# Performance work log

Measured on AMD Instinct MI355X. Metric: run time of the kernel, lower is better.

## Reference

```python
import jax, jax.numpy as jnp
import numpy as np

B, S, D, H, HD, F, V = 16, 512, 256, 8, 32, 682, 32000
EPS = 1.1920928955078125e-07


def rmsnorm(x, w):
    return x * jax.lax.rsqrt(jnp.mean(x * x, axis=-1, keepdims=True) + EPS) * w


def rope(x, cos, sin):
    # interleaved RoPE: even/odd lanes rotated pairwise, re-interleaved
    xe, xo = x[..., ::2], x[..., 1::2]
    return jnp.stack([xe * cos - xo * sin, xe * sin + xo * cos], axis=-1).reshape(x.shape)


def setup_inputs() -> dict:
    key = jax.random.key(0)
    ks = jax.random.split(key, 12)
    def n(k, shape, s=0.02):
        return jax.random.normal(k, shape, jnp.float32) * s
    pos = jnp.arange(S, dtype=jnp.float32)
    inv = 1.0 / (10000.0 ** (jnp.arange(0, HD, 2, dtype=jnp.float32) / HD))
    ang = pos[:, None] * inv[None, :]                      # [S, HD/2]
    cos_tab = jnp.repeat(jnp.cos(ang), 2, axis=-1)         # [S, HD]
    sin_tab = jnp.repeat(jnp.sin(ang), 2, axis=-1)
    mask = jnp.tril(jnp.ones((S, S), jnp.int32))[None, None]  # causal [1,1,S,S]
    return dict(
        emb=n(ks[0], (V, D)),
        pos_emb=n(ks[1], (S, D)),
        attn_norm_w=jnp.ones((D,), jnp.float32),
        wq=n(ks[2], (D, D)), bq=jnp.zeros((D,), jnp.float32),
        wk=n(ks[3], (HD, D)), bk=jnp.zeros((HD,), jnp.float32),
        wv=n(ks[4], (D, D)), bv=jnp.zeros((D,), jnp.float32),
        cos_tab=cos_tab, sin_tab=sin_tab,
        ffn_norm_w=jnp.ones((D,), jnp.float32),
        w_gate=n(ks[5], (F, D)), b_gate=jnp.zeros((F,), jnp.float32),
        w_up=n(ks[6], (F, D)), b_up=jnp.zeros((F,), jnp.float32),
        w_down=n(ks[7], (D, F)), b_down=jnp.zeros((D,), jnp.float32),
        tok_ids=jax.random.randint(ks[8], (B, S), 0, V, jnp.int64),
        mask=mask,
    )


def reference(emb, pos_emb, attn_norm_w, wq, bq, wk, bk, wv, bv, cos_tab, sin_tab,
              ffn_norm_w, w_gate, b_gate, w_up, b_up, w_down, b_down, tok_ids, mask):
    h = emb[tok_ids] + pos_emb                                   # [B,S,D]
    x = rmsnorm(h, attn_norm_w)
    # faithful to trace: direct view [B,S,D] -> [B,H,S,HD] (no transpose)
    q = (x @ wq.T + bq).reshape(B, H, S, HD)
    k = (x @ wk.T + bk)[:, None]                                 # [B,1,S,HD] single KV head
    v = (x @ wv.T + bv).reshape(B, H, S, HD)
    cos = cos_tab[:S, ::2][None, None]                           # [1,1,S,HD/2]
    sin = sin_tab[:S, ::2][None, None]
    qr = rope(q, cos, sin)
    kr = rope(k, cos, sin)[:, 0]                                 # [B,S,HD]
    scores = jnp.einsum('bhsd,btd->bhst', qr, kr) / jnp.sqrt(jnp.float32(HD))
    scores = jnp.where(mask == 0, -jnp.inf, scores)
    attn = jax.nn.softmax(scores, axis=-1)
    o = jnp.einsum('bhst,bhtd->bhsd', attn, v).reshape(B, S, D)
    h2 = o + h
    x2 = rmsnorm(h2, ffn_norm_w)
    g = x2 @ w_gate.T + b_gate
    g = g * jax.nn.sigmoid(g)                                    # SiLU gate
    up = x2 @ w_up.T + b_up
    out = (g * up) @ w_down.T + b_down
    # faithful to trace: residual uses post-norm activation x2, not h2
    return out + x2
```

## Files before the change

### kernel.cpp

```cpp
#include <hip/hip_runtime.h>
#include <hip/hip_bf16.h>
#include <cstddef>
#include <cstdint>

constexpr int Bb = 16, Ss = 512, Dd = 256, Hh = 8, HDd = 32, Ff = 682;
constexpr int FKp = 704;
constexpr float EPSf = 1.1920928955078125e-07f;

typedef short bf8v __attribute__((ext_vector_type(8)));
typedef float f4 __attribute__((ext_vector_type(4)));
using bf16 = __hip_bfloat16;

__device__ inline f4 MFMA(bf8v a, bf8v b, f4 c) {
  return __builtin_amdgcn_mfma_f32_16x16x32_bf16(a, b, c, 0, 0, 0);
}

__device__ __forceinline__ void gl_lds16(const bf16* g, bf16* l) {
  __builtin_amdgcn_global_load_lds(
      (const __attribute__((address_space(1))) unsigned int*)(g),
      (__attribute__((address_space(3))) unsigned int*)(l), 16, 0, 0);
}

__global__ __launch_bounds__(256) void k_prep(
    const float* __restrict__ wq, const float* __restrict__ wk,
    const float* __restrict__ wv, const float* __restrict__ wg,
    const float* __restrict__ wu, const float* __restrict__ wd,
    bf16* __restrict__ dqkv, bf16* __restrict__ dgate,
    bf16* __restrict__ dup, bf16* __restrict__ ddown,
    const float* __restrict__ emb, const float* __restrict__ pos,
    const int* __restrict__ tok, const float* __restrict__ w,
    bf16* __restrict__ hb, bf16* __restrict__ xb)
{
  const int b = blockIdx.x, tid = threadIdx.x;
  if (b < 640) {
    const int idx = b * 256 + tid;
    const int row = idx >> 8, col = idx & 255;
    float v;
    if (row < 256)      v = wq[(size_t)row * 256 + col];
    else if (row < 288) v = wk[(size_t)(row - 256) * 256 + col];
    else if (row < 544) v = wv[(size_t)(row - 288) * 256 + col];
    else                v = 0.f;
    dqkv[idx] = __float2bfloat16(v);
  } else if (b < 2176) {
    const bool isg = b < 1408;
    const int idx = (b - (isg ? 640 : 1408)) * 256 + tid;
    const int row = idx >> 8, col = idx & 255;
    const float* src = isg ? wg : wu;
    float v = (row < Ff) ? src[(size_t)row * 256 + col] : 0.f;
    (isg ? dgate : dup)[idx] = __float2bfloat16(v);
  } else if (b < 2880) {
    const int idx = (b - 2176) * 256 + tid;
    const int row = idx / FKp, col = idx - row * FKp;
    float v = (col < Ff) ? wd[(size_t)row * Ff + col] : 0.f;
    ddown[idx] = __float2bfloat16(v);
  } else {
    const int row = b - 2880;
    const int s = row & (Ss - 1);
    const int t = tok[row];
    float v = emb[(size_t)t * Dd + tid] + pos[(size_t)s * Dd + tid];
    float ss = v * v;
    #pragma unroll
    for (int off = 32; off > 0; off >>= 1) ss += __shfl_down(ss, off);
    __shared__ float red[4];
    if ((tid & 63) == 0) red[tid >> 6] = ss;
    __syncthreads();
    const float tot = red[0] + red[1] + red[2] + red[3];
    const float r = rsqrtf(tot * (1.0f / Dd) + EPSf);
    const size_t o = (size_t)row * Dd + tid;
    hb[o] = __float2bfloat16(v);
    xb[o] = __float2bfloat16(v * r * w[tid]);
  }
}

__global__ __launch_bounds__(256) void k_add_norm(
    const bf16* __restrict__ a, const bf16* __restrict__ hb,
    const float* __restrict__ w, bf16* __restrict__ x2b)
{
  const int row = blockIdx.x;
  const int tid = threadIdx.x;
  const size_t off = (size_t)row * Dd + tid;
  const float v = __bfloat162float(a[off]) + __bfloat162float(hb[off]);
  float ss = v * v;
  #pragma unroll
  for (int o = 32; o > 0; o >>= 1) ss += __shfl_down(ss, o);
  __shared__ float red[4];
  if ((tid & 63) == 0) red[tid >> 6] = ss;
  __syncthreads();
  const float tot = red[0] + red[1] + red[2] + red[3];
  const float r = rsqrtf(tot * (1.0f / Dd) + EPSf);
  x2b[off] = __float2bfloat16(v * r * w[tid]);
}

__global__ __launch_bounds__(256) void k_qkv(
    const bf16* __restrict__ A, const bf16* __restrict__ W,
    const float* __restrict__ bias0, const float* __restrict__ bias1,
    const float* __restrict__ bias2,
    const float* __restrict__ cost, const float* __restrict__ sint,
    bf16* __restrict__ ob0, bf16* __restrict__ ob1, bf16* __restrict__ vt)
{
  __shared__ bf16 As[128 * 64];
  __shared__ bf16 Bs[64 * 64];
  const int tid = threadIdx.x, lane = tid & 63, wv = tid >> 6;
  const int l15 = lane & 15, lg = lane >> 4;
  const int m0 = blockIdx.x * 128, n0 = blockIdx.y * 64;
  const int wr = (wv >> 1) * 64, wc = (wv & 1) * 32;
  const int sr8 = lane >> 3, slot = lane & 7;

  f4 acc[4][2];
  #pragma unroll
  for (int i = 0; i < 4; i++)
    #pragma unroll
    for (int j = 0; j < 2; j++) acc[i][j] = (f4){0.f, 0.f, 0.f, 0.f};

  for (int ks = 0; ks < 4; ks++) {
    const int k0 = ks * 64;
    #pragma unroll
    for (int i = 0; i < 4; i++) {
      const int row = wv * 32 + i * 8 + sr8;
      gl_lds16(&A[(size_t)(m0 + row) * 256 + k0 + slot * 8],
               &As[(wv * 32 + i * 8) * 64]);
    }
    #pragma unroll
    for (int i = 0; i < 2; i++) {
      const int row = wv * 16 + i * 8 + sr8;
      gl_lds16(&W[(size_t)(n0 + row) * 256 + k0 + slot * 8],
               &Bs[(wv * 16 + i * 8) * 64]);
    }
    __syncthreads();
    #pragma unroll
    for (int kk = 0; kk < 64; kk += 32) {
      bf8v af[4], bw[2];
      #pragma unroll
      for (int mi = 0; mi < 4; mi++)
        af[mi] = *(const bf8v*)&As[(wr + mi * 16 + l15) * 64 + kk + lg * 8];
      #pragma unroll
      for (int ni = 0; ni < 2; ni++)
        bw[ni] = *(const bf8v*)&Bs[(wc + ni * 16 + l15) * 64 + kk + lg * 8];
      #pragma unroll
      for (int mi = 0; mi < 4; mi++)
        #pragma unroll
        for (int ni = 0; ni < 2; ni++)
          acc[mi][ni] = MFMA(af[mi], bw[ni], acc[mi][ni]);
    }
    if (ks < 3) __syncthreads();
  }

  #pragma unroll
  for (int mi = 0; mi < 4; mi++) {
    #pragma unroll
    for (int ni = 0; ni < 2; ni++) {
      const int nbase = n0 + wc + ni * 16;
      const int n = nbase + l15;
      if (nbase < 288) {
        #pragma unroll
        for (int r = 0; r < 4; r++) {
          const int m = m0 + wr + mi * 16 + lg * 4 + r;
          float vb2 = acc[mi][ni][r] + (nbase < 256 ? bias0[n] : bias1[n - 256]);
          int s, hd;
          if (nbase < 256) { const int flat = ((m & 511) << 8) + n; s = (flat >> 5) & 511; hd = n & 31; }
          else             { s = m & 511; hd = n - 256; }
          const float c = cost[s * 32 + hd], sn = sint[s * 32 + hd];
          const float other = __shfl_xor(vb2, 1);
          const float res = (n & 1) ? (other * sn + vb2 * c) : (vb2 * c - other * sn);
          if (nbase < 256) ob0[(size_t)m * 256 + n] = __float2bfloat16(res);
          else             ob1[(size_t)m * 32 + hd] = __float2bfloat16(res);
        }
      } else if (nbase < 544) {
        const int rel = n - 288;
        const int hd = rel & 31, rq = rel >> 5;
        const int mb = m0 + wr + mi * 16 + lg * 4;
        const int b = mb >> 9;
        const float bv = bias2[rel];
        #pragma unroll
        for (int r = 0; r < 4; r++) {
          const int s = (mb + r) & 511;
          const int hh2 = s >> 6;
          const int s4 = ((s & 63) << 3) + rq;
          vt[((size_t)(b * Hh + hh2) * HDd + hd) * Ss + s4] =
              __float2bfloat16(acc[mi][ni][r] + bv);
        }
      }
    }
  }
}

__global__ __launch_bounds__(256) void k_ffn(
    const bf16* __restrict__ A, const bf16* __restrict__ Wg,
    const bf16* __restrict__ Wu,
    const float* __restrict__ bg, const float* __restrict__ bu,
    bf16* __restrict__ out)
{
  __shared__ bf16 As[128 * 64];
  __shared__ bf16 Gs[64 * 64];
  __shared__ bf16 Us[64 * 64];
  const int tid = threadIdx.x, lane = tid & 63, wv = tid >> 6;
  const int l15 = lane & 15, lg = lane >> 4;
  const int m0 = blockIdx.x * 128, n0 = blockIdx.y * 64;
  const int wr = (wv >> 1) * 64, wc = (wv & 1) * 32;
  const int sr8 = lane >> 3, slot = lane & 7;

  f4 accg[4][2], accu[4][2];
  #pragma unroll
  for (int i = 0; i < 4; i++)
    #pragma unroll
    for (int j = 0; j < 2; j++) {
      accg[i][j] = (f4){0.f, 0.f, 0.f, 0.f};
      accu[i][j] = (f4){0.f, 0.f, 0.f, 0.f};
    }

  for (int ks = 0; ks < 4; ks++) {
    const int k0 = ks * 64;
    #pragma unroll
    for (int i = 0; i < 4; i++) {
      const int row = wv * 32 + i * 8 + sr8;
      gl_lds16(&A[(size_t)(m0 + row) * 256 + k0 + slot * 8],
               &As[(wv * 32 + i * 8) * 64]);
    }
    #pragma unroll
    for (int i = 0; i < 2; i++) {
      const int row = wv * 16 + i * 8 + sr8;
      gl_lds16(&Wg[(size_t)(n0 + row) * 256 + k0 + slot * 8],
               &Gs[(wv * 16 + i * 8) * 64]);
      gl_lds16(&Wu[(size_t)(n0 + row) * 256 + k0 + slot * 8],
               &Us[(wv * 16 + i * 8) * 64]);
    }
    __syncthreads();
    #pragma unroll
    for (int kk = 0; kk < 64; kk += 32) {
      bf8v af[4], bgf[2], buf[2];
      #pragma unroll
      for (int mi = 0; mi < 4; mi++)
        af[mi] = *(const bf8v*)&As[(wr + mi * 16 + l15) * 64 + kk + lg * 8];
      #pragma unroll
      for (int ni = 0; ni < 2; ni++) {
        bgf[ni] = *(const bf8v*)&Gs[(wc + ni * 16 + l15) * 64 + kk + lg * 8];
        buf[ni] = *(const bf8v*)&Us[(wc + ni * 16 + l15) * 64 + kk + lg * 8];
      }
      #pragma unroll
      for (int mi = 0; mi < 4; mi++)
        #pragma unroll
        for (int ni = 0; ni < 2; ni++) {
          accg[mi][ni] = MFMA(af[mi], bgf[ni], accg[mi][ni]);
          accu[mi][ni] = MFMA(af[mi], buf[ni], accu[mi][ni]);
        }
    }
    if (ks < 3) __syncthreads();
  }

  #pragma unroll
  for (int ni = 0; ni < 2; ni++) {
    const int n = n0 + wc + ni * 16 + l15;
    const float bgv = (n < Ff) ? bg[n] : 0.f;
    const float buv = (n < Ff) ? bu[n] : 0.f;
    #pragma unroll
    for (int mi = 0; mi < 4; mi++) {
      #pragma unroll
      for (int r = 0; r < 4; r++) {
        const int m = m0 + wr + mi * 16 + lg * 4 + r;
        float res = 0.f;
        if (n < Ff) {
          const float gv = accg[mi][ni][r] + bgv;
          const float uv = accu[mi][ni][r] + buv;
          res = gv / (1.f + __expf(-gv)) * uv;
        }
        out[(size_t)m * FKp + n] = __float2bfloat16(res);
      }
    }
  }
}

__global__ __launch_bounds__(256) void k_down(
    const bf16* __restrict__ A, const bf16* __restrict__ W,
    const float* __restrict__ bias, const bf16* __restrict__ resid,
    float* __restrict__ out)
{
  __shared__ bf16 As[64 * 64];
  __shared__ bf16 Bs[64 * 64];
  const int tid = threadIdx.x, lane = tid & 63, wv = tid >> 6;
  const int l15 = lane & 15, lg = lane >> 4;
  const int m0 = blockIdx.x * 64, n0 = blockIdx.y * 64;
  const int wr = (wv >> 1) * 32, wc = (wv & 1) * 32;
  const int sr8 = lane >> 3, slot = lane & 7;

  f4 acc[2][2];
  #pragma unroll
  for (int i = 0; i < 2; i++)
    #pragma unroll
    for (int j = 0; j < 2; j++) acc[i][j] = (f4){0.f, 0.f, 0.f, 0.f};

  for (int ks = 0; ks < 11; ks++) {
    const int k0 = ks * 64;
    #pragma unroll
    for (int i = 0; i < 2; i++) {
      const int rowa = wv * 16 + i * 8 + sr8;
      gl_lds16(&A[(size_t)(m0 + rowa) * FKp + k0 + slot * 8],
               &As[(wv * 16 + i * 8) * 64]);
      gl_lds16(&W[(size_t)(n0 + rowa) * FKp + k0 + slot * 8],
               &Bs[(wv * 16 + i * 8) * 64]);
    }
    __syncthreads();
    #pragma unroll
    for (int kk = 0; kk < 64; kk += 32) {
      bf8v af[2], bw[2];
      #pragma unroll
      for (int mi = 0; mi < 2; mi++)
        af[mi] = *(const bf8v*)&As[(wr + mi * 16 + l15) * 64 + kk + lg * 8];
      #pragma unroll
      for (int ni = 0; ni < 2; ni++)
        bw[ni] = *(const bf8v*)&Bs[(wc + ni * 16 + l15) * 64 + kk + lg * 8];
      #pragma unroll
      for (int mi = 0; mi < 2; mi++)
        #pragma unroll
        for (int ni = 0; ni < 2; ni++)
          acc[mi][ni] = MFMA(af[mi], bw[ni], acc[mi][ni]);
    }
    if (ks < 10) __syncthreads();
  }

  #pragma unroll
  for (int ni = 0; ni < 2; ni++) {
    const int n = n0 + wc + ni * 16 + l15;
    const float bv = bias[n];
    #pragma unroll
    for (int mi = 0; mi < 2; mi++) {
      #pragma unroll
      for (int r = 0; r < 4; r++) {
        const int m = m0 + wr + mi * 16 + lg * 4 + r;
        out[(size_t)m * 256 + n] = acc[mi][ni][r] + bv +
            __bfloat162float(resid[(size_t)m * 256 + n]);
      }
    }
  }
}

__global__ __launch_bounds__(64) void k_attn_mfma(
    const bf16* __restrict__ q, const bf16* __restrict__ k,
    const bf16* __restrict__ vt, bf16* __restrict__ o)
{
  __shared__ bf16 Ps[16 * 72];
  const int lane = threadIdx.x;
  const int l15 = lane & 15, lg = lane >> 4;
  const int hh = blockIdx.y, bb = blockIdx.z;
  const int bh = bb * Hh + hh;
  const int qrow = (31 - blockIdx.x) * 16;
  const int lt = (qrow + 15) >> 6;
  const float scale = 0.17677669529663687f;

  const bf16* kg = k + (size_t)bb * Ss * HDd;
  const bf16* vg = vt + (size_t)bh * (Ss * HDd);

  const bf8v qf = *(const bf8v*)&q[((size_t)bh * Ss + qrow + l15) * HDd + lg * 8];

  f4 oacc[2];
  oacc[0] = (f4){0.f, 0.f, 0.f, 0.f};
  oacc[1] = (f4){0.f, 0.f, 0.f, 0.f};
  float m = -3.0e38f, l = 0.f;

  for (int ti = 0; ti <= lt; ti++) {
    const int t0 = ti * 64;

    f4 sf[4];
    __builtin_amdgcn_s_setprio(1);
    #pragma unroll
    for (int tf = 0; tf < 4; tf++) {
      const bf8v kf = *(const bf8v*)&kg[(size_t)(t0 + tf * 16 + l15) * HDd + lg * 8];
      sf[tf] = MFMA(kf, qf, (f4){0.f, 0.f, 0.f, 0.f});
    }
    __builtin_amdgcn_s_setprio(0);

    bf8v vb[2][2];
    #pragma unroll
    for (int kt = 0; kt < 2; kt++)
      #pragma unroll
      for (int hf = 0; hf < 2; hf++)
        vb[kt][hf] = *(const bf8v*)&vg[(size_t)(hf * 16 + l15) * Ss + t0 + kt * 32 + lg * 8];

    float pm = -3.0e38f;
    if (ti == lt) {
      #pragma unroll
      for (int tf = 0; tf < 4; tf++)
        #pragma unroll
        for (int r = 0; r < 4; r++) {
          float sv = sf[tf][r] * scale;
          if (t0 + tf * 16 + lg * 4 + r > qrow + l15) sv = -3.0e38f;
          sf[tf][r] = sv;
          pm = fmaxf(pm, sv);
        }
    } else {
      #pragma unroll
      for (int tf = 0; tf < 4; tf++)
        #pragma unroll
        for (int r = 0; r < 4; r++) {
          const float sv = sf[tf][r] * scale;
          sf[tf][r] = sv;
          pm = fmaxf(pm, sv);
        }
    }
    pm = fmaxf(pm, __shfl_xor(pm, 16));
    pm = fmaxf(pm, __shfl_xor(pm, 32));

    const float nm = fmaxf(m, pm);
    const float corr = __expf(m - nm);
    m = nm;

    float ls = 0.f;
    #pragma unroll
    for (int tf = 0; tf < 4; tf++)
      #pragma unroll
      for (int r = 0; r < 4; r++) {
        const float p = __expf(sf[tf][r] - m);
        sf[tf][r] = p;
        ls += p;
      }
    ls += __shfl_xor(ls, 16);
    ls += __shfl_xor(ls, 32);
    l = l * corr + ls;

    #pragma unroll
    for (int tf = 0; tf < 4; tf++) {
      bf16 t4[4];
      #pragma unroll
      for (int r = 0; r < 4; r++) t4[r] = __float2bfloat16(sf[tf][r]);
      *(uint2*)&Ps[l15 * 72 + tf * 16 + lg * 4] = *(const uint2*)t4;
    }

    float corrT[4];
    #pragma unroll
    for (int r = 0; r < 4; r++) corrT[r] = __shfl(corr, lg * 4 + r);
    #pragma unroll
    for (int hf = 0; hf < 2; hf++)
      #pragma unroll
      for (int r = 0; r < 4; r++) oacc[hf][r] *= corrT[r];

    __builtin_amdgcn_s_setprio(1);
    #pragma unroll
    for (int kt = 0; kt < 2; kt++) {
      const bf8v pv = *(const bf8v*)&Ps[l15 * 72 + kt * 32 + lg * 8];
      #pragma unroll
      for (int hf = 0; hf < 2; hf++)
        oacc[hf] = MFMA(pv, vb[kt][hf], oacc[hf]);
    }
    __builtin_amdgcn_s_setprio(0);
  }

  float lT[4];
  #pragma unroll
  for (int r = 0; r < 4; r++) lT[r] = __shfl(l, lg * 4 + r);
  #pragma unroll
  for (int hf = 0; hf < 2; hf++)
    #pragma unroll
    for (int r = 0; r < 4; r++)
      o[((size_t)bh * Ss + qrow + lg * 4 + r) * HDd + hf * 16 + l15] =
          __float2bfloat16(oacc[hf][r] / lT[r]);
}

extern "C" void kernel_launch(void* const* d_in, const int* in_sizes, int n_in,
                              void* d_out, int out_size, void* d_ws, size_t ws_size,
                              hipStream_t stream)
{
  const float* emb     = (const float*)d_in[0];
  const float* pos_emb = (const float*)d_in[1];
  const float* attn_w  = (const float*)d_in[2];
  const float* wq      = (const float*)d_in[3];
  const float* bq      = (const float*)d_in[4];
  const float* wk      = (const float*)d_in[5];
  const float* bk      = (const float*)d_in[6];
  const float* wv      = (const float*)d_in[7];
  const float* bv      = (const float*)d_in[8];
  const float* cos_t   = (const float*)d_in[9];
  const float* sin_t   = (const float*)d_in[10];
  const float* ffn_w   = (const float*)d_in[11];
  const float* w_gate  = (const float*)d_in[12];
  const float* b_gate  = (const float*)d_in[13];
  const float* w_up    = (const float*)d_in[14];
  const float* b_up    = (const float*)d_in[15];
  const float* w_down  = (const float*)d_in[16];
  const float* b_down  = (const float*)d_in[17];
  const int*   tok     = (const int*)d_in[18];
  float* out = (float*)d_out;

  const size_t NT = (size_t)Bb * Ss;
  char* base = (char*)d_ws;
  size_t off = 0;
  auto alloc = [&](size_t bytes) {
    void* r = base + off;
    off = (off + bytes + 255) & ~(size_t)255;
    return r;
  };
  bf16*  h_bf   = (bf16*)alloc(NT * Dd * 2);
  bf16*  x_bf   = (bf16*)alloc(NT * Dd * 2);
  bf16*  q_bf   = (bf16*)alloc(NT * Dd * 2);
  bf16*  k_bf   = (bf16*)alloc(NT * HDd * 2);
  bf16*  vt_bf  = (bf16*)alloc(NT * Dd * 2);
  bf16*  o_bf   = (bf16*)alloc(NT * Dd * 2);
  bf16*  x2_bf  = (bf16*)alloc(NT * Dd * 2);
  bf16*  g_bf   = (bf16*)alloc(NT * (size_t)FKp * 2);
  bf16*  wqkv_b = (bf16*)alloc((size_t)640 * 256 * 2);
  bf16*  wgate_b= (bf16*)alloc((size_t)768 * 256 * 2);
  bf16*  wup_b  = (bf16*)alloc((size_t)768 * 256 * 2);
  bf16*  wdown_b= (bf16*)alloc((size_t)256 * FKp * 2);

  k_prep<<<dim3(2880 + NT), 256, 0, stream>>>(
      wq, wk, wv, w_gate, w_up, w_down, wqkv_b, wgate_b, wup_b, wdown_b,
      emb, pos_emb, tok, attn_w, h_bf, x_bf);

  k_qkv<<<dim3(NT / 128, 10), 256, 0, stream>>>(
      x_bf, wqkv_b, bq, bk, bv, cos_t, sin_t, q_bf, k_bf, vt_bf);

  k_attn_mfma<<<dim3(32, Hh, Bb), 64, 0, stream>>>(q_bf, k_bf, vt_bf, o_bf);

  k_add_norm<<<dim3(NT), 256, 0, stream>>>(o_bf, h_bf, ffn_w, x2_bf);

  k_ffn<<<dim3(NT / 128, 11), 256, 0, stream>>>(
      x2_bf, wgate_b, wup_b, b_gate, b_up, g_bf);

  k_down<<<dim3(NT / 64, 4), 256, 0, stream>>>(
      g_bf, wdown_b, b_down, x2_bf, out);
}
```

Before: 90.74 us.

## Double-buffer LDS tiles in GEMM kernels and shrink FFN M-tile

Adds two-stage LDS double buffering to the qkv, ffn and down GEMM kernels, so the global-to-LDS load of the next K slice is issued before the MFMAs on the current slice, hiding load latency. The FFN kernel's M tile also shrinks from 128 to 64 rows, doubling its grid for better occupancy and wave count. The cost is more LDS per block and, in the FFN kernel, less reuse of the weight tiles. Synchronisation relies on the barrier at the end of each iteration, which also covers the asynchronous LDS loads.

Result: slower. 96.58 us (+6.4%).

```diff
diff --git a/kernel.cpp b/kernel.cpp
--- a/kernel.cpp
+++ b/kernel.cpp
@@ -98,44 +98,46 @@
     const float* __restrict__ cost, const float* __restrict__ sint,
     bf16* __restrict__ ob0, bf16* __restrict__ ob1, bf16* __restrict__ vt)
 {
-  __shared__ bf16 As[128 * 64];
-  __shared__ bf16 Bs[64 * 64];
+  __shared__ bf16 As[2][128 * 64];
+  __shared__ bf16 Bs[2][64 * 64];
   const int tid = threadIdx.x, lane = tid & 63, wv = tid >> 6;
   const int l15 = lane & 15, lg = lane >> 4;
   const int m0 = blockIdx.x * 128, n0 = blockIdx.y * 64;
   const int wr = (wv >> 1) * 64, wc = (wv & 1) * 32;
   const int sr8 = lane >> 3, slot = lane & 7;
 
+  auto stage = [&](int ks, int buf) {
+    const int k0 = ks * 64;
+    #pragma unroll
+    for (int i = 0; i < 4; i++)
+      gl_lds16(&A[(size_t)(m0 + wv * 32 + i * 8 + sr8) * 256 + k0 + slot * 8],
+               &As[buf][(wv * 32 + i * 8) * 64]);
+    #pragma unroll
+    for (int i = 0; i < 2; i++)
+      gl_lds16(&W[(size_t)(n0 + wv * 16 + i * 8 + sr8) * 256 + k0 + slot * 8],
+               &Bs[buf][(wv * 16 + i * 8) * 64]);
+  };
+
   f4 acc[4][2];
   #pragma unroll
   for (int i = 0; i < 4; i++)
     #pragma unroll
     for (int j = 0; j < 2; j++) acc[i][j] = (f4){0.f, 0.f, 0.f, 0.f};
 
+  stage(0, 0);
+  __syncthreads();
   for (int ks = 0; ks < 4; ks++) {
-    const int k0 = ks * 64;
-    #pragma unroll
-    for (int i = 0; i < 4; i++) {
-      const int row = wv * 32 + i * 8 + sr8;
-      gl_lds16(&A[(size_t)(m0 + row) * 256 + k0 + slot * 8],
-               &As[(wv * 32 + i * 8) * 64]);
-    }
-    #pragma unroll
-    for (int i = 0; i < 2; i++) {
-      const int row = wv * 16 + i * 8 + sr8;
-      gl_lds16(&W[(size_t)(n0 + row) * 256 + k0 + slot * 8],
-               &Bs[(wv * 16 + i * 8) * 64]);
-    }
-    __syncthreads();
+    const int cur = ks & 1;
+    if (ks < 3) stage(ks + 1, cur ^ 1);
     #pragma unroll
     for (int kk = 0; kk < 64; kk += 32) {
       bf8v af[4], bw[2];
       #pragma unroll
       for (int mi = 0; mi < 4; mi++)
-        af[mi] = *(const bf8v*)&As[(wr + mi * 16 + l15) * 64 + kk + lg * 8];
+        af[mi] = *(const bf8v*)&As[cur][(wr + mi * 16 + l15) * 64 + kk + lg * 8];
       #pragma unroll
       for (int ni = 0; ni < 2; ni++)
-        bw[ni] = *(const bf8v*)&Bs[(wc + ni * 16 + l15) * 64 + kk + lg * 8];
+        bw[ni] = *(const bf8v*)&Bs[cur][(wc + ni * 16 + l15) * 64 + kk + lg * 8];
       #pragma unroll
       for (int mi = 0; mi < 4; mi++)
         #pragma unroll
@@ -190,58 +192,58 @@
     const float* __restrict__ bg, const float* __restrict__ bu,
     bf16* __restrict__ out)
 {
-  __shared__ bf16 As[128 * 64];
-  __shared__ bf16 Gs[64 * 64];
-  __shared__ bf16 Us[64 * 64];
+  __shared__ bf16 As[2][64 * 64];
+  __shared__ bf16 Gs[2][64 * 64];
+  __shared__ bf16 Us[2][64 * 64];
   const int tid = threadIdx.x, lane = tid & 63, wv = tid >> 6;
   const int l15 = lane & 15, lg = lane >> 4;
-  const int m0 = blockIdx.x * 128, n0 = blockIdx.y * 64;
-  const int wr = (wv >> 1) * 64, wc = (wv & 1) * 32;
+  const int m0 = blockIdx.x * 64, n0 = blockIdx.y * 64;
+  const int wr = (wv >> 1) * 32, wc = (wv & 1) * 32;
   const int sr8 = lane >> 3, slot = lane & 7;
 
-  f4 accg[4][2], accu[4][2];
-  #pragma unroll
-  for (int i = 0; i < 4; i++)
+  auto stage = [&](int ks, int buf) {
+    const int k0 = ks * 64;
+    #pragma unroll
+    for (int i = 0; i < 2; i++) {
+      const int row = wv * 16 + i * 8 + sr8;
+      const int loff = (wv * 16 + i * 8) * 64;
+      gl_lds16(&A[(size_t)(m0 + row) * 256 + k0 + slot * 8], &As[buf][loff]);
+      gl_lds16(&Wg[(size_t)(n0 + row) * 256 + k0 + slot * 8], &Gs[buf][loff]);
+      gl_lds16(&Wu[(size_t)(n0 + row) * 256 + k0 + slot * 8], &Us[buf][loff]);
+    }
+  };
+
+  f4 accg[2][2], accu[2][2];
+  #pragma unroll
+  for (int i = 0; i < 2; i++)
     #pragma unroll
     for (int j = 0; j < 2; j++) {
       accg[i][j] = (f4){0.f, 0.f, 0.f, 0.f};
       accu[i][j] = (f4){0.f, 0.f, 0.f, 0.f};
     }
 
+  stage(0, 0);
+  __syncthreads();
   for (int ks = 0; ks < 4; ks++) {
-    const int k0 = ks * 64;
-    #pragma unroll
-    for (int i = 0; i < 4; i++) {
-      const int row = wv * 32 + i * 8 + sr8;
-      gl_lds16(&A[(size_t)(m0 + row) * 256 + k0 + slot * 8],
-               &As[(wv * 32 + i * 8) * 64]);
-    }
-    #pragma unroll
-    for (int i = 0; i < 2; i++) {
-      const int row = wv * 16 + i * 8 + sr8;
-      gl_lds16(&Wg[(size_t)(n0 + row) * 256 + k0 + slot * 8],
-               &Gs[(wv * 16 + i * 8) * 64]);
-      gl_lds16(&Wu[(size_t)(n0 + row) * 256 + k0 + slot * 8],
-               &Us[(wv * 16 + i * 8) * 64]);
-    }
-    __syncthreads();
+    const int cur = ks & 1;
+    if (ks < 3) stage(ks + 1, cur ^ 1);
     #pragma unroll
     for (int kk = 0; kk < 64; kk += 32) {
-      bf8v af[4], bgf[2], buf[2];
-      #pragma unroll
-      for (int mi = 0; mi < 4; mi++)
-        af[mi] = *(const bf8v*)&As[(wr + mi * 16 + l15) * 64 + kk + lg * 8];
+      bf8v af[2], bgf[2], buf2[2];
+      #pragma unroll
+      for (int mi = 0; mi < 2; mi++)
+        af[mi] = *(const bf8v*)&As[cur][(wr + mi * 16 + l15) * 64 + kk + lg * 8];
       #pragma unroll
       for (int ni = 0; ni < 2; ni++) {
-        bgf[ni] = *(const bf8v*)&Gs[(wc + ni * 16 + l15) * 64 + kk + lg * 8];
-        buf[ni] = *(const bf8v*)&Us[(wc + ni * 16 + l15) * 64 + kk + lg * 8];
+        bgf[ni] = *(const bf8v*)&Gs[cur][(wc + ni * 16 + l15) * 64 + kk + lg * 8];
+        buf2[ni] = *(const bf8v*)&Us[cur][(wc + ni * 16 + l15) * 64 + kk + lg * 8];
       }
       #pragma unroll
-      for (int mi = 0; mi < 4; mi++)
+      for (int mi = 0; mi < 2; mi++)
         #pragma unroll
         for (int ni = 0; ni < 2; ni++) {
           accg[mi][ni] = MFMA(af[mi], bgf[ni], accg[mi][ni]);
-          accu[mi][ni] = MFMA(af[mi], buf[ni], accu[mi][ni]);
+          accu[mi][ni] = MFMA(af[mi], buf2[ni], accu[mi][ni]);
         }
     }
     if (ks < 3) __syncthreads();
@@ -253,7 +255,7 @@
     const float bgv = (n < Ff) ? bg[n] : 0.f;
     const float buv = (n < Ff) ? bu[n] : 0.f;
     #pragma unroll
-    for (int mi = 0; mi < 4; mi++) {
+    for (int mi = 0; mi < 2; mi++) {
       #pragma unroll
       for (int r = 0; r < 4; r++) {
         const int m = m0 + wr + mi * 16 + lg * 4 + r;
@@ -274,40 +276,45 @@
     const float* __restrict__ bias, const bf16* __restrict__ resid,
     float* __restrict__ out)
 {
-  __shared__ bf16 As[64 * 64];
-  __shared__ bf16 Bs[64 * 64];
+  __shared__ bf16 As[2][64 * 64];
+  __shared__ bf16 Bs[2][64 * 64];
   const int tid = threadIdx.x, lane = tid & 63, wv = tid >> 6;
   const int l15 = lane & 15, lg = lane >> 4;
   const int m0 = blockIdx.x * 64, n0 = blockIdx.y * 64;
   const int wr = (wv >> 1) * 32, wc = (wv & 1) * 32;
   const int sr8 = lane >> 3, slot = lane & 7;
 
+  auto stage = [&](int ks, int buf) {
+    const int k0 = ks * 64;
+    #pragma unroll
+    for (int i = 0; i < 2; i++) {
+      const int row = wv * 16 + i * 8 + sr8;
+      const int loff = (wv * 16 + i * 8) * 64;
+      gl_lds16(&A[(size_t)(m0 + row) * FKp + k0 + slot * 8], &As[buf][loff]);
+      gl_lds16(&W[(size_t)(n0 + row) * FKp + k0 + slot * 8], &Bs[buf][loff]);
+    }
+  };
+
   f4 acc[2][2];
   #pragma unroll
   for (int i = 0; i < 2; i++)
     #pragma unroll
     for (int j = 0; j < 2; j++) acc[i][j] = (f4){0.f, 0.f, 0.f, 0.f};
 
+  stage(0, 0);
+  __syncthreads();
   for (int ks = 0; ks < 11; ks++) {
-    const int k0 = ks * 64;
-    #pragma unroll
-    for (int i = 0; i < 2; i++) {
-      const int rowa = wv * 16 + i * 8 + sr8;
-      gl_lds16(&A[(size_t)(m0 + rowa) * FKp + k0 + slot * 8],
-               &As[(wv * 16 + i * 8) * 64]);
-      gl_lds16(&W[(size_t)(n0 + rowa) * FKp + k0 + slot * 8],
-               &Bs[(wv * 16 + i * 8) * 64]);
-    }
-    __syncthreads();
+    const int cur = ks & 1;
+    if (ks < 10) stage(ks + 1, cur ^ 1);
     #pragma unroll
     for (int kk = 0; kk < 64; kk += 32) {
       bf8v af[2], bw[2];
       #pragma unroll
       for (int mi = 0; mi < 2; mi++)
-        af[mi] = *(const bf8v*)&As[(wr + mi * 16 + l15) * 64 + kk + lg * 8];
+        af[mi] = *(const bf8v*)&As[cur][(wr + mi * 16 + l15) * 64 + kk + lg * 8];
       #pragma unroll
       for (int ni = 0; ni < 2; ni++)
-        bw[ni] = *(const bf8v*)&Bs[(wc + ni * 16 + l15) * 64 + kk + lg * 8];
+        bw[ni] = *(const bf8v*)&Bs[cur][(wc + ni * 16 + l15) * 64 + kk + lg * 8];
       #pragma unroll
       for (int mi = 0; mi < 2; mi++)
         #pragma unroll
@@ -511,7 +518,7 @@
 
   k_add_norm<<<dim3(NT), 256, 0, stream>>>(o_bf, h_bf, ffn_w, x2_bf);
 
-  k_ffn<<<dim3(NT / 128, 11), 256, 0, stream>>>(
+  k_ffn<<<dim3(NT / 64, 11), 256, 0, stream>>>(
       x2_bf, wgate_b, wup_b, b_gate, b_up, g_bf);
 
   k_down<<<dim3(NT / 64, 4), 256, 0, stream>>>(
```
